# Performance work log

Hardware: AMD Instinct MI355X
Metric: run time of the kernel (lower is better)

Reference implementation:

```python
import jax, jax.numpy as jnp
import numpy as np

D_MODEL = 128
NUM_LAYERS = 2
D_FF = 512
VOCAB = 128
OUT_DIM = 10
B, S = 512, 256
EPS_FEAT = 1e-6
LN_EPS = 1e-5


def _pos_encoding(seq_len, d):
    pos = jnp.arange(seq_len, dtype=jnp.float32)[:, None]            # [S,1]
    div = jnp.exp(jnp.arange(0, d, 2, dtype=jnp.float32) * (-np.log(10000.0) / d))
    ang = pos * div                                                   # [S,D/2]
    pe = jnp.stack([jnp.sin(ang), jnp.cos(ang)], axis=-1).reshape(seq_len, d)
    return pe[:, None, :]                                             # [S,1,D]


def _layer_norm(x, g, b):
    mu = jnp.mean(x, axis=-1, keepdims=True)
    var = jnp.mean(jnp.square(x - mu), axis=-1, keepdims=True)
    return (x - mu) * jax.lax.rsqrt(var + LN_EPS) * g + b


def setup_inputs() -> dict:
    key = jax.random.key(0)
    ks = jax.random.split(key, 20)
    sc = 0.02
    inp = {
        'src': jax.random.randint(ks[0], (B, S), 0, VOCAB),
        'emb': jax.random.normal(ks[1], (VOCAB, D_MODEL), jnp.float32) * sc,
        'wq': jax.random.normal(ks[2], (NUM_LAYERS, D_MODEL, D_MODEL), jnp.float32) * sc,
        'bq': jnp.zeros((NUM_LAYERS, D_MODEL), jnp.float32),
        'wk': jax.random.normal(ks[3], (NUM_LAYERS, D_MODEL, D_MODEL), jnp.float32) * sc,
        'bk': jnp.zeros((NUM_LAYERS, D_MODEL), jnp.float32),
        'wv': jax.random.normal(ks[4], (NUM_LAYERS, D_MODEL, D_MODEL), jnp.float32) * sc,
        'bv': jnp.zeros((NUM_LAYERS, D_MODEL), jnp.float32),
        'w1': jax.random.normal(ks[5], (NUM_LAYERS, D_FF, D_MODEL), jnp.float32) * sc,
        'b1': jnp.zeros((NUM_LAYERS, D_FF), jnp.float32),
        'w2': jax.random.normal(ks[6], (NUM_LAYERS, D_MODEL, D_FF), jnp.float32) * sc,
        'b2': jnp.zeros((NUM_LAYERS, D_MODEL), jnp.float32),
        'g1': jnp.ones((NUM_LAYERS, D_MODEL), jnp.float32),
        'beta1': jnp.zeros((NUM_LAYERS, D_MODEL), jnp.float32),
        'g2': jnp.ones((NUM_LAYERS, D_MODEL), jnp.float32),
        'beta2': jnp.zeros((NUM_LAYERS, D_MODEL), jnp.float32),
        'fc_w': jax.random.normal(ks[7], (OUT_DIM, D_MODEL), jnp.float32) * sc,
        'fc_b': jnp.zeros((OUT_DIM,), jnp.float32),
    }
    return inp


def reference(src, emb, wq, bq, wk, bk, wv, bv, w1, b1, w2, b2,
              g1, beta1, g2, beta2, fc_w, fc_b):
    # src: [B,S] int -> permute -> [S,B]
    x = emb[src.T] * np.sqrt(float(D_MODEL))          # [S,B,D]
    x = x + _pos_encoding(x.shape[0], D_MODEL)
    for l in range(NUM_LAYERS):
        # Linear attention (faithful to original: einsum 'b' axis = seq here)
        Q = jax.nn.relu(jnp.einsum('sbd,ed->sbe', x, wq[l]) + bq[l]) + EPS_FEAT
        K = jax.nn.relu(jnp.einsum('sbd,ed->sbe', x, wk[l]) + bk[l]) + EPS_FEAT
        V = jnp.einsum('sbd,ed->sbe', x, wv[l]) + bv[l]
        KV = jnp.einsum('snd,sne->sde', K, V)         # [S,D,D] (n = batch axis)
        Z = 1.0 / (jnp.einsum('snd,sd->sn', Q, K.sum(axis=1)) + EPS_FEAT)  # [S,B]
        attn = jnp.einsum('snd,sde,sn->sne', Q, KV, Z)  # [S,B,D]
        x = _layer_norm(x + attn, g1[l], beta1[l])
        ff = jnp.einsum('sbf,df->sbd',
                        jax.nn.relu(jnp.einsum('sbd,fd->sbf', x, w1[l]) + b1[l]),
                        w2[l]) + b2[l]
        x = _layer_norm(x + ff, g2[l], beta2[l])
    x = jnp.transpose(x, (1, 0, 2))                   # [B,S,D]
    pooled = jnp.mean(x, axis=1)                      # [B,D]
    return pooled @ fc_w.T + fc_b                     # [B,OUT]
```

## Files before the change

### kernel.cpp

```cpp
#include <hip/hip_runtime.h>

typedef unsigned short u16;
typedef unsigned int u32;
typedef short bf16x8 __attribute__((ext_vector_type(8)));
typedef float f32x4 __attribute__((ext_vector_type(4)));

__device__ __forceinline__ float b2f(u16 v) { return __uint_as_float(((u32)v) << 16); }
__device__ __forceinline__ u16 f2b(float f) {
    u32 x = __float_as_uint(f);
    return (u16)((x + 0x7fffu + ((x >> 16) & 1u)) >> 16);
}

__device__ __forceinline__ void gld_lds16(const u16* g, u16* l) {
    __builtin_amdgcn_global_load_lds(
        (const __attribute__((address_space(1))) unsigned int*)g,
        (__attribute__((address_space(3))) unsigned int*)l,
        16, 0, 0);
}

#define S_LEN 256
#define B_SZ  512
#define DM    128
#define DFF   512
#define MROWS (S_LEN * B_SZ)

__device__ __forceinline__ int sw16(int r, int d) {
    return r * 128 + ((((d >> 3) ^ (r & 15)) & 15) << 3) + (d & 7);
}

__global__ __launch_bounds__(256) void detect_kernel(const u32* __restrict__ embw,
                                                     int* __restrict__ flag) {
    int z = 0, big = 0;
    for (int i = threadIdx.x; i < 8192; i += 256) {
        u32 w = embw[i];
        u32 lo = w & 0xffffu;
        if (lo == 0u) z++;
        else if (((lo >> 7) & 0xffu) >= 0xC0u) big++;
    }
#pragma unroll
    for (int off = 32; off > 0; off >>= 1) {
        z   += __shfl_xor(z, off, 64);
        big += __shfl_xor(big, off, 64);
    }
    __shared__ int zz[4], bb[4];
    if ((threadIdx.x & 63) == 0) { zz[threadIdx.x >> 6] = z; bb[threadIdx.x >> 6] = big; }
    __syncthreads();
    if (threadIdx.x == 0) {
        int Z = zz[0] + zz[1] + zz[2] + zz[3];
        int Bc = bb[0] + bb[1] + bb[2] + bb[3];
        flag[0] = (Z > 4096 || Bc > 16) ? 1 : 0;
    }
}

struct Ptrs { const void* p[17]; };

__global__ __launch_bounds__(256) void convert_kernel(Ptrs ps, u16* __restrict__ canon,
                                                      const int* __restrict__ flag) {
    const int cnt[17] = {16384,32768,256,32768,256,32768,256,131072,1024,131072,
                         256,256,256,256,256,1280,10};
    const int off[17] = {0,16384,49152,49408,82176,82432,115200,115456,246528,
                         247552,378624,378880,379136,379392,379648,379904,381184};
    const int bst[18] = {0,8,24,25,41,42,58,59,123,124,188,189,190,191,192,193,194,195};
    const int isf = *flag;
    const int blk = blockIdx.x;
    int idx = 0;
#pragma unroll
    for (int i = 0; i < 17; ++i) if (blk >= bst[i + 1]) idx = i + 1;
    const int local = blk - bst[idx];
    const int n = cnt[idx];
    const void* sp = ps.p[idx];
    u16* dp = canon + off[idx];
#pragma unroll
    for (int j = 0; j < 8; ++j) {
        int e = local * 2048 + j * 256 + threadIdx.x;
        if (e < n) {
            u16 v = isf ? f2b(((const float*)sp)[e]) : ((const u16*)sp)[e];
            dp[e] = v;
        }
    }
}

__global__ __launch_bounds__(256) void pe_kernel(float* __restrict__ PE) {
    int idx = blockIdx.x * 256 + threadIdx.x;
    int s = idx >> 6, d2 = idx & 63;
    float ang = (float)s * expf((float)(d2 * 2) * -0.0719557841560639f);
    float2 sc; sc.x = sinf(ang); sc.y = cosf(ang);
    *(float2*)(PE + s * DM + d2 * 2) = sc;
}

__global__ __launch_bounds__(256) void embed_kernel(const int* __restrict__ src,
                                                    const u16* __restrict__ emb,
                                                    const float* __restrict__ PE,
                                                    u16* __restrict__ X) {
    int idx = blockIdx.x * 256 + threadIdx.x;
    int dq = idx & 15;
    int m = idx >> 4;
    int s = m >> 9;
    int b = m & 511;
    int tok = src[b * S_LEN + s];
    int d = dq * 8;
    uint4 ev = *(const uint4*)(emb + tok * DM + d);
    const float* pe = PE + s * DM + d;
    u16 o[8];
    const u32 ew[4] = {ev.x, ev.y, ev.z, ev.w};
#pragma unroll
    for (int p = 0; p < 4; ++p) {
        float e0 = __uint_as_float((ew[p] & 0xffffu) << 16) * 11.3137084989847604f;
        float e1 = __uint_as_float(ew[p] & 0xffff0000u)     * 11.3137084989847604f;
        o[p * 2]     = f2b(e0 + pe[p * 2]);
        o[p * 2 + 1] = f2b(e1 + pe[p * 2 + 1]);
    }
    uint4 wv;
    wv.x = (u32)o[0] | ((u32)o[1] << 16);
    wv.y = (u32)o[2] | ((u32)o[3] << 16);
    wv.z = (u32)o[4] | ((u32)o[5] << 16);
    wv.w = (u32)o[6] | ((u32)o[7] << 16);
    *(uint4*)(X + (size_t)m * DM + d) = wv;
}

__global__ __launch_bounds__(256) void kvproj_kernel(
    const u16* __restrict__ X, const u16* __restrict__ Wk, const u16* __restrict__ bk,
    const u16* __restrict__ Wv, const u16* __restrict__ bv,
    u16* __restrict__ KVt, float* __restrict__ Ksum)
{
    __shared__ __align__(16) char sm_[49152];
    u16* Xs = (u16*)sm_;
    u16* Kt = (u16*)(sm_ + 16384);
    u16* Vt = (u16*)(sm_ + 32768);
    const int s = blockIdx.x, t = threadIdx.x;
    const int w = t >> 6, quad = (t >> 4) & 3, lr = t & 15;
    const int l = t & 63;
    const u16* Xg = X + (size_t)s * B_SZ * DM;

#define STAGE_XS(B0)                                                            \
    {                                                                           \
        _Pragma("unroll")                                                       \
        for (int i = 0; i < 4; ++i) {                                           \
            int r = w * 16 + i * 4 + (l >> 4);                                  \
            int ss = (l & 15) ^ (r & 15);                                       \
            gld_lds16(Xg + (size_t)((B0) + r) * DM + (ss << 3),                 \
                      Xs + w * 2048 + i * 512);                                 \
        }                                                                       \
    }

    bf16x8 wkf[2][4], wvf[2][4];
    float kb[2], vb[2];
#pragma unroll
    for (int ct = 0; ct < 2; ++ct) {
        int e = w * 32 + ct * 16 + lr;
#pragma unroll
        for (int kc = 0; kc < 4; ++kc) {
            wkf[ct][kc] = *(const bf16x8*)(Wk + e * 128 + kc * 32 + quad * 8);
            wvf[ct][kc] = *(const bf16x8*)(Wv + e * 128 + kc * 32 + quad * 8);
        }
        kb[ct] = b2f(bk[e]);
        vb[ct] = b2f(bv[e]);
    }

    const f32x4 z4 = {0.f, 0.f, 0.f, 0.f};
    f32x4 kvacc[2][8];
#pragma unroll
    for (int dt = 0; dt < 2; ++dt)
#pragma unroll
        for (int ct = 0; ct < 8; ++ct) kvacc[dt][ct] = z4;
    float ks[2] = {0.f, 0.f};

    STAGE_XS(0)
    __syncthreads();

    for (int b0 = 0; b0 < B_SZ; b0 += 64) {
        f32x4 pa[4][2];
#pragma unroll
        for (int mt = 0; mt < 4; ++mt) { pa[mt][0] = z4; pa[mt][1] = z4; }
#pragma unroll
        for (int kc = 0; kc < 4; ++kc) {
            bf16x8 a[4];
#pragma unroll
            for (int mt = 0; mt < 4; ++mt)
                a[mt] = *(const bf16x8*)(Xs + sw16(mt * 16 + lr, kc * 32 + quad * 8));
#pragma unroll
            for (int ct = 0; ct < 2; ++ct)
#pragma unroll
                for (int mt = 0; mt < 4; ++mt)
                    pa[mt][ct] = __builtin_amdgcn_mfma_f32_16x16x32_bf16(a[mt], wkf[ct][kc], pa[mt][ct], 0, 0, 0);
        }
#pragma unroll
        for (int ct = 0; ct < 2; ++ct) {
            int e = w * 32 + ct * 16 + lr, e7 = e & 7;
#pragma unroll
            for (int mt = 0; mt < 4; ++mt) {
                u16 h[4]; float ssum = 0.f;
#pragma unroll
                for (int j = 0; j < 4; ++j) {
                    float v = fmaxf(pa[mt][ct][j] + kb[ct], 0.f) + 1e-6f;
                    h[j] = f2b(v); ssum += b2f(h[j]);
                }
                ks[ct] += ssum;
                uint2 pk; pk.x = (u32)h[0] | ((u32)h[1] << 16); pk.y = (u32)h[2] | ((u32)h[3] << 16);
                int bs = mt * 2 + (quad >> 1);
                *(uint2*)(Kt + e * 64 + (((bs ^ e7) & 7) << 3) + (quad & 1) * 4) = pk;
            }
        }
#pragma unroll
        for (int mt = 0; mt < 4; ++mt) { pa[mt][0] = z4; pa[mt][1] = z4; }
#pragma unroll
        for (int kc = 0; kc < 4; ++kc) {
            bf16x8 a[4];
#pragma unroll
            for (int mt = 0; mt < 4; ++mt)
                a[mt] = *(const bf16x8*)(Xs + sw16(mt * 16 + lr, kc * 32 + quad * 8));
#pragma unroll
            for (int ct = 0; ct < 2; ++ct)
#pragma unroll
                for (int mt = 0; mt < 4; ++mt)
                    pa[mt][ct] = __builtin_amdgcn_mfma_f32_16x16x32_bf16(a[mt], wvf[ct][kc], pa[mt][ct], 0, 0, 0);
        }
#pragma unroll
        for (int ct = 0; ct < 2; ++ct) {
            int e = w * 32 + ct * 16 + lr, e7 = e & 7;
#pragma unroll
            for (int mt = 0; mt < 4; ++mt) {
                u16 h[4];
#pragma unroll
                for (int j = 0; j < 4; ++j) h[j] = f2b(pa[mt][ct][j] + vb[ct]);
                uint2 pk; pk.x = (u32)h[0] | ((u32)h[1] << 16); pk.y = (u32)h[2] | ((u32)h[3] << 16);
                int bs = mt * 2 + (quad >> 1);
                *(uint2*)(Vt + e * 64 + (((bs ^ e7) & 7) << 3) + (quad & 1) * 4) = pk;
            }
        }
        __syncthreads();
        if (b0 < B_SZ - 64) STAGE_XS(b0 + 64)
#pragma unroll
        for (int kc = 0; kc < 2; ++kc) {
            bf16x8 ka[2];
#pragma unroll
            for (int dt = 0; dt < 2; ++dt) {
                int d = (2 * w + dt) * 16 + lr;
                ka[dt] = *(const bf16x8*)(Kt + d * 64 + ((((kc * 4 + quad) ^ (d & 7)) & 7) << 3));
            }
#pragma unroll
            for (int ct = 0; ct < 8; ++ct) {
                int e = ct * 16 + lr;
                bf16x8 vf = *(const bf16x8*)(Vt + e * 64 + ((((kc * 4 + quad) ^ (e & 7)) & 7) << 3));
                kvacc[0][ct] = __builtin_amdgcn_mfma_f32_16x16x32_bf16(ka[0], vf, kvacc[0][ct], 0, 0, 0);
                kvacc[1][ct] = __builtin_amdgcn_mfma_f32_16x16x32_bf16(ka[1], vf, kvacc[1][ct], 0, 0, 0);
            }
        }
        __syncthreads();
    }
#undef STAGE_XS
#pragma unroll
    for (int ct = 0; ct < 2; ++ct) {
        float v = ks[ct];
        v += __shfl_xor(v, 16, 64);
        v += __shfl_xor(v, 32, 64);
        if (quad == 0) Ksum[s * 128 + w * 32 + ct * 16 + lr] = v;
    }
    u16* KVg = KVt + (size_t)s * (DM * DM);
#pragma unroll
    for (int dt = 0; dt < 2; ++dt) {
        int d0 = (2 * w + dt) * 16 + quad * 4;
#pragma unroll
        for (int ct = 0; ct < 8; ++ct) {
            int e = ct * 16 + lr;
            u16 h[4];
#pragma unroll
            for (int j = 0; j < 4; ++j) h[j] = f2b(kvacc[dt][ct][j]);
            uint2 pk; pk.x = (u32)h[0] | ((u32)h[1] << 16); pk.y = (u32)h[2] | ((u32)h[3] << 16);
            *(uint2*)(KVg + e * 128 + d0) = pk;
        }
    }
}

__global__ __launch_bounds__(256) void attn_ln_kernel(
    const u16* X, const u16* __restrict__ Wq, const u16* __restrict__ bq,
    const u16* __restrict__ KVt, const float* __restrict__ Ksum,
    u16* Xout, const u16* __restrict__ g, const u16* __restrict__ beta)
{
    __shared__ __align__(16) char sm_[65536];
    u16* R1 = (u16*)sm_;
    u16* R2 = (u16*)(sm_ + 32768);
    const int blk = blockIdx.x, s = blk >> 2, rc = blk & 3, t = threadIdx.x;
    const int w = t >> 6, quad = (t >> 4) & 3, lr = t & 15;
    const int l = t & 63;
    const size_t m0 = (size_t)s * B_SZ + rc * 128;

#pragma unroll
    for (int i = 0; i < 8; ++i) {
        int r = w * 32 + i * 4 + (l >> 4);
        int ss = (l & 15) ^ (r & 15);
        gld_lds16(Wq + (size_t)r * DM + (ss << 3), R1 + w * 4096 + i * 512);
        gld_lds16(X + (m0 + r) * DM + (ss << 3),   R2 + w * 4096 + i * 512);
    }
    __syncthreads();
    const f32x4 z4 = {0.f, 0.f, 0.f, 0.f};
    f32x4 qacc[2][8];
#pragma unroll
    for (int mt = 0; mt < 2; ++mt)
#pragma unroll
        for (int ct = 0; ct < 8; ++ct) qacc[mt][ct] = z4;
#pragma unroll
    for (int kc = 0; kc < 4; ++kc) {
        bf16x8 a[2];
#pragma unroll
        for (int mt = 0; mt < 2; ++mt)
            a[mt] = *(const bf16x8*)(R2 + sw16(w * 32 + mt * 16 + lr, kc * 32 + quad * 8));
#pragma unroll
        for (int ct = 0; ct < 8; ++ct) {
            bf16x8 wf = *(const bf16x8*)(R1 + sw16(ct * 16 + lr, kc * 32 + quad * 8));
            qacc[0][ct] = __builtin_amdgcn_mfma_f32_16x16x32_bf16(a[0], wf, qacc[0][ct], 0, 0, 0);
            qacc[1][ct] = __builtin_amdgcn_mfma_f32_16x16x32_bf16(a[1], wf, qacc[1][ct], 0, 0, 0);
        }
    }
    __syncthreads();
    const u16* KVg = KVt + (size_t)s * (DM * DM);
#pragma unroll
    for (int i = 0; i < 8; ++i) {
        int e = w * 32 + i * 4 + (l >> 4);
        int ss = (l & 15) ^ (e & 15);
        gld_lds16(KVg + (size_t)e * DM + (ss << 3), R2 + w * 4096 + i * 512);
    }
    float ksm[8], bqv[8];
#pragma unroll
    for (int ct = 0; ct < 8; ++ct) {
        ksm[ct] = Ksum[s * 128 + ct * 16 + lr];
        bqv[ct] = b2f(bq[ct * 16 + lr]);
    }
    float zden[2][4];
#pragma unroll
    for (int mt = 0; mt < 2; ++mt)
#pragma unroll
        for (int j = 0; j < 4; ++j) zden[mt][j] = 0.f;
#pragma unroll
    for (int mt = 0; mt < 2; ++mt)
#pragma unroll
        for (int ct = 0; ct < 8; ++ct) {
            int d = ct * 16 + lr;
#pragma unroll
            for (int j = 0; j < 4; ++j) {
                float qv = fmaxf(qacc[mt][ct][j] + bqv[ct], 0.f) + 1e-6f;
                u16 qb16 = f2b(qv);
                zden[mt][j] += b2f(qb16) * ksm[ct];
                int b = w * 32 + mt * 16 + quad * 4 + j;
                R1[sw16(b, d)] = qb16;
            }
        }
#pragma unroll
    for (int mt = 0; mt < 2; ++mt)
#pragma unroll
        for (int j = 0; j < 4; ++j) {
            float v = zden[mt][j];
            v += __shfl_xor(v, 1, 64); v += __shfl_xor(v, 2, 64);
            v += __shfl_xor(v, 4, 64); v += __shfl_xor(v, 8, 64);
            zden[mt][j] = 1.f / (v + 1e-6f);
        }
    __syncthreads();
    f32x4 oacc[2][8];
#pragma unroll
    for (int mt = 0; mt < 2; ++mt)
#pragma unroll
        for (int ct = 0; ct < 8; ++ct) oacc[mt][ct] = z4;
#pragma unroll
    for (int kc = 0; kc < 4; ++kc) {
        bf16x8 qa[2];
#pragma unroll
        for (int mt = 0; mt < 2; ++mt)
            qa[mt] = *(const bf16x8*)(R1 + sw16(w * 32 + mt * 16 + lr, kc * 32 + quad * 8));
#pragma unroll
        for (int ct = 0; ct < 8; ++ct) {
            bf16x8 kf = *(const bf16x8*)(R2 + sw16(ct * 16 + lr, kc * 32 + quad * 8));
            oacc[0][ct] = __builtin_amdgcn_mfma_f32_16x16x32_bf16(qa[0], kf, oacc[0][ct], 0, 0, 0);
            oacc[1][ct] = __builtin_amdgcn_mfma_f32_16x16x32_bf16(qa[1], kf, oacc[1][ct], 0, 0, 0);
        }
    }
    float gv[8], bev[8];
#pragma unroll
    for (int ct = 0; ct < 8; ++ct) {
        gv[ct]  = b2f(g[ct * 16 + lr]);
        bev[ct] = b2f(beta[ct * 16 + lr]);
    }
#pragma unroll
    for (int mt = 0; mt < 2; ++mt)
#pragma unroll
        for (int j = 0; j < 4; ++j) {
            int b = w * 32 + mt * 16 + quad * 4 + j;
            const u16* xr = X + (m0 + b) * DM;
            float vals[8], sum = 0.f, sq = 0.f;
#pragma unroll
            for (int ct = 0; ct < 8; ++ct) {
                float v = fmaf(oacc[mt][ct][j], zden[mt][j], b2f(xr[ct * 16 + lr]));
                vals[ct] = v; sum += v; sq += v * v;
            }
            sum += __shfl_xor(sum, 1, 64); sq += __shfl_xor(sq, 1, 64);
            sum += __shfl_xor(sum, 2, 64); sq += __shfl_xor(sq, 2, 64);
            sum += __shfl_xor(sum, 4, 64); sq += __shfl_xor(sq, 4, 64);
            sum += __shfl_xor(sum, 8, 64); sq += __shfl_xor(sq, 8, 64);
            float mean = sum * 0.0078125f;
            float var  = sq * 0.0078125f - mean * mean;
            float rstd = rsqrtf(fmaxf(var, 0.f) + 1e-5f);
            u16* xo = Xout + (m0 + b) * DM;
#pragma unroll
            for (int ct = 0; ct < 8; ++ct)
                xo[ct * 16 + lr] = f2b((vals[ct] - mean) * rstd * gv[ct] + bev[ct]);
        }
}

__global__ __launch_bounds__(256, 4) void mlp_kernel(
    const u16* X, const u16* __restrict__ W1, const u16* __restrict__ b1,
    const u16* __restrict__ W2, const u16* __restrict__ b2,
    u16* Xout, const u16* __restrict__ g, const u16* __restrict__ beta)
{
    __shared__ __align__(16) char sm_[40960];
    u16* W1c = (u16*)sm_;
    u16* W2c = (u16*)(sm_ + 16384);
    u16* Hc  = (u16*)(sm_ + 32768);
    const int t = threadIdx.x;
    const int m0 = blockIdx.x * 64;
    const int w  = t >> 6;
    const int quad = (t >> 4) & 3;
    const int lr = t & 15;
    const int l  = t & 63;

    bf16x8 af[4];
    {
        const u16* xr = X + (size_t)(m0 + w * 16 + lr) * DM + quad * 8;
#pragma unroll
        for (int kc = 0; kc < 4; ++kc)
            af[kc] = *(const bf16x8*)(xr + kc * 32);
    }

    const f32x4 zero4 = {0.f, 0.f, 0.f, 0.f};
    f32x4 zacc[8];
#pragma unroll
    for (int ct = 0; ct < 8; ++ct) zacc[ct] = zero4;

#define STAGE_W1(FC)                                                            \
    {                                                                           \
        _Pragma("unroll")                                                       \
        for (int i = 0; i < 4; ++i) {                                           \
            int r = w * 16 + i * 4 + (l >> 4);                                  \
            int sslot = (l & 15) ^ (r & 15);                                    \
            gld_lds16(W1 + (size_t)((FC) + r) * DM + (sslot << 3),              \
                      W1c + w * 2048 + i * 512);                                \
        }                                                                       \
    }
#define STAGE_W2(FC)                                                            \
    {                                                                           \
        _Pragma("unroll")                                                       \
        for (int i = 0; i < 4; ++i) {                                           \
            int d = w * 32 + i * 8 + (l >> 3);                                  \
            int sslot = (l & 7) ^ (d & 7);                                      \
            gld_lds16(W2 + (size_t)d * DFF + (FC) + (sslot << 3),               \
                      W2c + w * 2048 + i * 512);                                \
        }                                                                       \
    }

    STAGE_W1(0)
    STAGE_W2(0)
    __syncthreads();

    for (int fc = 0; fc < DFF; fc += 64) {
        f32x4 hacc[4];
#pragma unroll
        for (int ct = 0; ct < 4; ++ct) hacc[ct] = zero4;
#pragma unroll
        for (int kc = 0; kc < 4; ++kc)
#pragma unroll
            for (int ct = 0; ct < 4; ++ct) {
                bf16x8 bf_ = *(const bf16x8*)(W1c + sw16(ct * 16 + lr, kc * 32 + quad * 8));
                hacc[ct] = __builtin_amdgcn_mfma_f32_16x16x32_bf16(af[kc], bf_, hacc[ct], 0, 0, 0);
            }
        __syncthreads();
        if (fc < DFF - 64) STAGE_W1(fc + 64)
#pragma unroll
        for (int ct = 0; ct < 4; ++ct) {
            int f = ct * 16 + lr;
            float hbv = b2f(b1[fc + f]);
#pragma unroll
            for (int j = 0; j < 4; ++j) {
                int m = w * 16 + quad * 4 + j;
                float v = fmaxf(hacc[ct][j] + hbv, 0.f);
                Hc[m * 64 + ((((f >> 3) ^ (m & 7)) & 7) << 3) + (f & 7)] = f2b(v);
            }
        }
#pragma unroll
        for (int kc = 0; kc < 2; ++kc) {
            int m = w * 16 + lr;
            bf16x8 ha = *(const bf16x8*)(Hc + m * 64 + ((((kc * 4 + quad) ^ (m & 7)) & 7) << 3));
#pragma unroll
            for (int ct = 0; ct < 8; ++ct) {
                int d = ct * 16 + lr;
                bf16x8 wb = *(const bf16x8*)(W2c + d * 64 + ((((kc * 4 + quad) ^ (d & 7)) & 7) << 3));
                zacc[ct] = __builtin_amdgcn_mfma_f32_16x16x32_bf16(ha, wb, zacc[ct], 0, 0, 0);
            }
        }
        __syncthreads();
        if (fc < DFF - 64) STAGE_W2(fc + 64)
    }
#undef STAGE_W1
#undef STAGE_W2

    float gv[8], bev[8], bbv[8];
#pragma unroll
    for (int ct = 0; ct < 8; ++ct) {
        gv[ct]  = b2f(g[ct * 16 + lr]);
        bev[ct] = b2f(beta[ct * 16 + lr]);
        bbv[ct] = b2f(b2[ct * 16 + lr]);
    }
#pragma unroll
    for (int j = 0; j < 4; ++j) {
        int m = w * 16 + quad * 4 + j;
        const u16* xr = X + (size_t)(m0 + m) * DM;
        float vals[8], sum = 0.f, sq = 0.f;
#pragma unroll
        for (int ct = 0; ct < 8; ++ct) {
            float v = zacc[ct][j] + bbv[ct] + b2f(xr[ct * 16 + lr]);
            vals[ct] = v; sum += v; sq += v * v;
        }
        sum += __shfl_xor(sum, 1, 64); sq += __shfl_xor(sq, 1, 64);
        sum += __shfl_xor(sum, 2, 64); sq += __shfl_xor(sq, 2, 64);
        sum += __shfl_xor(sum, 4, 64); sq += __shfl_xor(sq, 4, 64);
        sum += __shfl_xor(sum, 8, 64); sq += __shfl_xor(sq, 8, 64);
        float mean = sum * 0.0078125f;
        float var  = sq * 0.0078125f - mean * mean;
        float rstd = rsqrtf(fmaxf(var, 0.f) + 1e-5f);
        u16* xo = Xout + (size_t)(m0 + m) * DM;
#pragma unroll
        for (int ct = 0; ct < 8; ++ct)
            xo[ct * 16 + lr] = f2b((vals[ct] - mean) * rstd * gv[ct] + bev[ct]);
    }
}

__global__ __launch_bounds__(128) void pool_fc_kernel(
    const u16* __restrict__ X, const u16* __restrict__ fcw,
    const u16* __restrict__ fcb, void* __restrict__ Out,
    const int* __restrict__ flag)
{
    __shared__ float pool[128];
    const int b = blockIdx.x, t = threadIdx.x;
    float acc = 0.f;
    for (int s = 0; s < S_LEN; ++s)
        acc += b2f(X[((size_t)s * B_SZ + b) * DM + t]);
    pool[t] = acc * (1.0f / 256.0f);
    __syncthreads();
    if (t < 10) {
        float o = b2f(fcb[t]);
        for (int d = 0; d < 128; ++d) o += pool[d] * b2f(fcw[t * 128 + d]);
        if (*flag) ((float*)Out)[b * 10 + t] = o;
        else       ((u16*)Out)[b * 10 + t] = f2b(o);
    }
}

extern "C" void kernel_launch(void* const* d_in, const int* in_sizes, int n_in,
                              void* d_out, int out_size, void* d_ws, size_t ws_size,
                              hipStream_t stream)
{
    const int* src = (const int*)d_in[0];

    char* ws = (char*)d_ws;
    u16*   X    = (u16*)ws;
    u16*   KVt  = (u16*)(ws + 33554432);
    float* Ksum = (float*)(ws + 41943040);
    int*   flag = (int*)(ws + 42074112);
    u16*   cn   = (u16*)(ws + 42074368);
    float* PE   = (float*)(ws + 33554432);

    u16* emb = cn + 0;
    u16* wq  = cn + 16384;
    u16* bq  = cn + 49152;
    u16* wk  = cn + 49408;
    u16* bk  = cn + 82176;
    u16* wv  = cn + 82432;
    u16* bvp = cn + 115200;
    u16* w1  = cn + 115456;
    u16* b1  = cn + 246528;
    u16* w2  = cn + 247552;
    u16* b2  = cn + 378624;
    u16* g1  = cn + 378880;
    u16* be1 = cn + 379136;
    u16* g2  = cn + 379392;
    u16* be2 = cn + 379648;
    u16* fcw = cn + 379904;
    u16* fcb = cn + 381184;

    detect_kernel<<<1, 256, 0, stream>>>((const u32*)d_in[1], flag);

    Ptrs ps;
    for (int i = 0; i < 17; ++i) ps.p[i] = d_in[i + 1];
    convert_kernel<<<195, 256, 0, stream>>>(ps, cn, flag);

    pe_kernel<<<64, 256, 0, stream>>>(PE);
    embed_kernel<<<MROWS * 16 / 256, 256, 0, stream>>>(src, emb, PE, X);

    for (int l = 0; l < 2; ++l) {
        kvproj_kernel<<<S_LEN, 256, 0, stream>>>(
            X, wk + l * DM * DM, bk + l * DM, wv + l * DM * DM, bvp + l * DM, KVt, Ksum);
        attn_ln_kernel<<<S_LEN * 4, 256, 0, stream>>>(
            X, wq + l * DM * DM, bq + l * DM, KVt, Ksum, X, g1 + l * DM, be1 + l * DM);
        mlp_kernel<<<MROWS / 64, 256, 0, stream>>>(
            X, w1 + l * DFF * DM, b1 + l * DFF, w2 + l * DM * DFF, b2 + l * DM,
            X, g2 + l * DM, be2 + l * DM);
    }

    pool_fc_kernel<<<B_SZ, 128, 0, stream>>>(X, fcw, fcb, d_out, flag);
}
```

Measured before the change: 365.4 us.

## Switch MLP kernel to 32x32x16 MFMA with 2x2 wave tiling and LDS-staged LayerNorm

Replaces the per-wave 16-row tiling of 16x16x32 MFMAs in the fused MLP kernel with a 2x2 wave grid of 32x32x16 MFMAs. Each wave now computes a 32-row by 32-column slice of the hidden layer and a 32x64 slice of the output. Because the output is split across waves, the accumulators are spilled to LDS (reusing the weight buffers) and LayerNorm is redone row-wise with a 64-lane shuffle reduction. The aim is fewer MFMA issues and fewer LDS B-operand reads. In exchange it adds an extra LDS round trip and a sync in the epilogue, and the hidden-tile stores come before the barrier.

```diff
diff --git a/kernel.cpp b/kernel.cpp
--- a/kernel.cpp
+++ b/kernel.cpp
@@ -4,6 +4,7 @@
 typedef unsigned int u32;
 typedef short bf16x8 __attribute__((ext_vector_type(8)));
 typedef float f32x4 __attribute__((ext_vector_type(4)));
+typedef float f32x16 __attribute__((ext_vector_type(16)));
 
 __device__ __forceinline__ float b2f(u16 v) { return __uint_as_float(((u32)v) << 16); }
 __device__ __forceinline__ u16 f2b(float f) {
@@ -414,25 +415,15 @@
     u16* W1c = (u16*)sm_;
     u16* W2c = (u16*)(sm_ + 16384);
     u16* Hc  = (u16*)(sm_ + 32768);
+    float* zs = (float*)sm_;
     const int t = threadIdx.x;
     const int m0 = blockIdx.x * 64;
     const int w  = t >> 6;
-    const int quad = (t >> 4) & 3;
-    const int lr = t & 15;
     const int l  = t & 63;
-
-    bf16x8 af[4];
-    {
-        const u16* xr = X + (size_t)(m0 + w * 16 + lr) * DM + quad * 8;
-#pragma unroll
-        for (int kc = 0; kc < 4; ++kc)
-            af[kc] = *(const bf16x8*)(xr + kc * 32);
-    }
-
-    const f32x4 zero4 = {0.f, 0.f, 0.f, 0.f};
-    f32x4 zacc[8];
-#pragma unroll
-    for (int ct = 0; ct < 8; ++ct) zacc[ct] = zero4;
+    const int l5 = l >> 5;
+    const int lc = l & 31;
+    const int mh = w >> 1;
+    const int fh = w & 1;
 
 #define STAGE_W1(FC)                                                            \
     {                                                                           \
@@ -455,43 +446,56 @@
         }                                                                       \
     }
 
+    bf16x8 af[8];
+    {
+        const u16* xr = X + (size_t)(m0 + mh * 32 + lc) * DM + l5 * 8;
+#pragma unroll
+        for (int ks = 0; ks < 8; ++ks)
+            af[ks] = *(const bf16x8*)(xr + ks * 16);
+    }
+
+    f32x16 zero16;
+#pragma unroll
+    for (int i = 0; i < 16; ++i) zero16[i] = 0.f;
+    f32x16 zacc0 = zero16, zacc1 = zero16;
+
     STAGE_W1(0)
     STAGE_W2(0)
     __syncthreads();
 
     for (int fc = 0; fc < DFF; fc += 64) {
-        f32x4 hacc[4];
-#pragma unroll
-        for (int ct = 0; ct < 4; ++ct) hacc[ct] = zero4;
-#pragma unroll
-        for (int kc = 0; kc < 4; ++kc)
-#pragma unroll
-            for (int ct = 0; ct < 4; ++ct) {
-                bf16x8 bf_ = *(const bf16x8*)(W1c + sw16(ct * 16 + lr, kc * 32 + quad * 8));
-                hacc[ct] = __builtin_amdgcn_mfma_f32_16x16x32_bf16(af[kc], bf_, hacc[ct], 0, 0, 0);
-            }
+        f32x16 hacc = zero16;
+#pragma unroll
+        for (int ks = 0; ks < 8; ++ks) {
+            bf16x8 bf_ = *(const bf16x8*)(W1c + sw16(fh * 32 + lc, ks * 16 + l5 * 8));
+            hacc = __builtin_amdgcn_mfma_f32_32x32x16_bf16(af[ks], bf_, hacc, 0, 0, 0);
+        }
+        {
+            float hbv = b2f(b1[fc + fh * 32 + lc]);
+            int f = fh * 32 + lc;
+#pragma unroll
+            for (int p = 0; p < 16; ++p) {
+                int m = mh * 32 + (p & 3) + 8 * (p >> 2) + 4 * l5;
+                float v = fmaxf(hacc[p] + hbv, 0.f);
+                Hc[m * 64 + ((((f >> 3) ^ (m & 7)) & 7) << 3) + (f & 7)] = f2b(v);
+            }
+        }
         __syncthreads();
         if (fc < DFF - 64) STAGE_W1(fc + 64)
 #pragma unroll
-        for (int ct = 0; ct < 4; ++ct) {
-            int f = ct * 16 + lr;
-            float hbv = b2f(b1[fc + f]);
-#pragma unroll
-            for (int j = 0; j < 4; ++j) {
-                int m = w * 16 + quad * 4 + j;
-                float v = fmaxf(hacc[ct][j] + hbv, 0.f);
-                Hc[m * 64 + ((((f >> 3) ^ (m & 7)) & 7) << 3) + (f & 7)] = f2b(v);
-            }
-        }
-#pragma unroll
-        for (int kc = 0; kc < 2; ++kc) {
-            int m = w * 16 + lr;
-            bf16x8 ha = *(const bf16x8*)(Hc + m * 64 + ((((kc * 4 + quad) ^ (m & 7)) & 7) << 3));
-#pragma unroll
-            for (int ct = 0; ct < 8; ++ct) {
-                int d = ct * 16 + lr;
-                bf16x8 wb = *(const bf16x8*)(W2c + d * 64 + ((((kc * 4 + quad) ^ (d & 7)) & 7) << 3));
-                zacc[ct] = __builtin_amdgcn_mfma_f32_16x16x32_bf16(ha, wb, zacc[ct], 0, 0, 0);
+        for (int ks = 0; ks < 4; ++ks) {
+            int f = ks * 16 + l5 * 8;
+            int m = mh * 32 + lc;
+            bf16x8 ha = *(const bf16x8*)(Hc + m * 64 + ((((f >> 3) ^ (m & 7)) & 7) << 3));
+            {
+                int d = (fh * 2) * 32 + lc;
+                bf16x8 wb = *(const bf16x8*)(W2c + d * 64 + ((((f >> 3) ^ (d & 7)) & 7) << 3));
+                zacc0 = __builtin_amdgcn_mfma_f32_32x32x16_bf16(ha, wb, zacc0, 0, 0, 0);
+            }
+            {
+                int d = (fh * 2 + 1) * 32 + lc;
+                bf16x8 wb = *(const bf16x8*)(W2c + d * 64 + ((((f >> 3) ^ (d & 7)) & 7) << 3));
+                zacc1 = __builtin_amdgcn_mfma_f32_32x32x16_bf16(ha, wb, zacc1, 0, 0, 0);
             }
         }
         __syncthreads();
@@ -500,34 +504,35 @@
 #undef STAGE_W1
 #undef STAGE_W2
 
-    float gv[8], bev[8], bbv[8];
-#pragma unroll
-    for (int ct = 0; ct < 8; ++ct) {
-        gv[ct]  = b2f(g[ct * 16 + lr]);
-        bev[ct] = b2f(beta[ct * 16 + lr]);
-        bbv[ct] = b2f(b2[ct * 16 + lr]);
-    }
-#pragma unroll
-    for (int j = 0; j < 4; ++j) {
-        int m = w * 16 + quad * 4 + j;
-        const u16* xr = X + (size_t)(m0 + m) * DM;
-        float vals[8], sum = 0.f, sq = 0.f;
-#pragma unroll
-        for (int ct = 0; ct < 8; ++ct) {
-            float v = zacc[ct][j] + bbv[ct] + b2f(xr[ct * 16 + lr]);
-            vals[ct] = v; sum += v; sq += v * v;
-        }
-        sum += __shfl_xor(sum, 1, 64); sq += __shfl_xor(sq, 1, 64);
-        sum += __shfl_xor(sum, 2, 64); sq += __shfl_xor(sq, 2, 64);
-        sum += __shfl_xor(sum, 4, 64); sq += __shfl_xor(sq, 4, 64);
-        sum += __shfl_xor(sum, 8, 64); sq += __shfl_xor(sq, 8, 64);
+    {
+        float b20 = b2f(b2[(fh * 2) * 32 + lc]);
+        float b21 = b2f(b2[(fh * 2 + 1) * 32 + lc]);
+#pragma unroll
+        for (int p = 0; p < 16; ++p) {
+            int mrow = mh * 32 + (p & 3) + 8 * (p >> 2) + 4 * l5;
+            zs[mrow * 128 + (fh * 2) * 32 + lc]     = zacc0[p] + b20;
+            zs[mrow * 128 + (fh * 2 + 1) * 32 + lc] = zacc1[p] + b21;
+        }
+    }
+    __syncthreads();
+
+    float g0 = b2f(g[l]), g1v = b2f(g[64 + l]);
+    float be0 = b2f(beta[l]), be1 = b2f(beta[64 + l]);
+    for (int q = 0; q < 16; ++q) {
+        int r = w * 16 + q;
+        float v0 = zs[r * 128 + l]      + b2f(X[(size_t)(m0 + r) * DM + l]);
+        float v1 = zs[r * 128 + 64 + l] + b2f(X[(size_t)(m0 + r) * DM + 64 + l]);
+        float sum = v0 + v1, sq = v0 * v0 + v1 * v1;
+#pragma unroll
+        for (int off = 32; off > 0; off >>= 1) {
+            sum += __shfl_xor(sum, off, 64);
+            sq  += __shfl_xor(sq,  off, 64);
+        }
         float mean = sum * 0.0078125f;
         float var  = sq * 0.0078125f - mean * mean;
         float rstd = rsqrtf(fmaxf(var, 0.f) + 1e-5f);
-        u16* xo = Xout + (size_t)(m0 + m) * DM;
-#pragma unroll
-        for (int ct = 0; ct < 8; ++ct)
-            xo[ct * 16 + lr] = f2b((vals[ct] - mean) * rstd * gv[ct] + bev[ct]);
+        Xout[(size_t)(m0 + r) * DM + l]      = f2b((v0 - mean) * rstd * g0  + be0);
+        Xout[(size_t)(m0 + r) * DM + 64 + l] = f2b((v1 - mean) * rstd * g1v + be1);
     }
 }
 
```

Measured after the change: 414.1 us. 1.13x slower.
